# Kernel optimization log

Hardware: AMD Instinct MI355X
Metric: run time of the kernel (lower is better)

The kernel has to match this reference:

```python
import jax, jax.numpy as jnp
import numpy as np

V, T, NS, NH, E, H = 4, 4, 100000, 12288, 100000, 64
NEG_SLOPE = 0.01  # nn.LeakyReLU default


def setup_inputs() -> dict:
    key = jax.random.key(0)
    k1, k2, k3, k4, k5 = jax.random.split(key, 5)
    x = jax.random.normal(k1, (V, T, NS), dtype=jnp.float32)          # per-var, per-t scalar node features
    src_idx = jax.random.randint(k2, (V, T, E), 0, NS, dtype=jnp.int32)
    dst_idx = jax.random.randint(k3, (V, T, E), 0, NH, dtype=jnp.int32)
    W = jax.random.normal(k4, (V, T, H), dtype=jnp.float32)            # GraphConv weight, in_feats=1 -> [1,H] per etype
    b = jax.random.normal(k5, (V, T, H), dtype=jnp.float32) * 0.02     # GraphConv bias per etype
    return {"x": x, "W": W, "b": b, "src_idx": src_idx, "dst_idx": dst_idx, "n_healpix": NH}


def reference(x, W, b, src_idx, dst_idx, n_healpix):
    # x: [V,T,NS]; W,b: [V,T,H]; src_idx,dst_idx: [V,T,E]
    x = jnp.nan_to_num(x, nan=0.0)

    def conv_scalar(x_v, src, dst):
        # x_v: [T,NS] (all timestep features for this var), src/dst: [E] for ONE edge type
        ones = jnp.ones(src.shape, x_v.dtype)
        deg_out = jax.ops.segment_sum(ones, src, num_segments=NS)       # out-degree of src nodes
        deg_in = jax.ops.segment_sum(ones, dst, num_segments=n_healpix)  # in-degree of dst nodes
        norm_src = jax.lax.rsqrt(jnp.maximum(deg_out, 1.0))
        norm_dst = jax.lax.rsqrt(jnp.maximum(deg_in, 1.0))
        msg = x_v[:, src] * norm_src[src]                                # [T,E] gather
        agg = jax.vmap(lambda m: jax.ops.segment_sum(m, dst, num_segments=n_healpix))(msg)  # [T,NH]
        return agg * norm_dst                                            # norm='both'

    # HeteroGraphConv bug-faithful: for each var, EVERY per-t' conv is applied to each x[:,t]
    # s[v, t', t, n] = normalized scatter of x[v,t] through edges of etype t'
    s = jax.vmap(lambda xv, sv, dv: jax.vmap(lambda se, de: conv_scalar(xv, se, de))(sv, dv))(
        x, src_idx, dst_idx)                                             # [V,T',T,NH]

    # in_feats=1: linear is outer product with W row; bias + LeakyReLU inside each conv, sum over etypes t'
    h = jax.nn.leaky_relu(s[..., None] * W[:, :, None, None, :] + b[:, :, None, None, :],
                          negative_slope=NEG_SLOPE)                      # [V,T',T,NH,H]
    out = h.sum(axis=1)                                                  # aggregate='sum' over edge types -> [V,T,NH,H]
    # final stacking: stack over t (dim=1) then over vars (dim=1) -> [NH, V, T, H]
    return jnp.transpose(out, (2, 0, 1, 3))
```

## Files before the change

### kernel.cpp

```cpp
#include <hip/hip_runtime.h>
#include <math.h>

#define V    4
#define T    4
#define NSRC 100000
#define NHX  12288
#define E    100000
#define H    64
#define VT   16

#define SL    16
#define SLE   (E/SL)
#define HF    8
#define HE    (E/HF)
#define CW    (NSRC/8)
#define LDSW  12500
#define NCH   12
#define NPB   8

#define S1_TRANS  391
#define S1_CNT    (HF*VT)
#define S1_DHIST  (SL*VT)
#define S2_SCAN   (NCH*VT)
#define S2_NSFIN  ((VT*CW + 1023)/1024)

typedef float vf4 __attribute__((ext_vector_type(4)));

__global__ void __launch_bounds__(1024)
s1_kernel(const float* __restrict__ x, const int* __restrict__ src,
          const int* __restrict__ dst, float4* __restrict__ x4,
          unsigned int* __restrict__ cnt_part, unsigned char* __restrict__ ph8,
          unsigned int* __restrict__ cs) {
    __shared__ unsigned int lds[LDSW];
    const int b = blockIdx.x, tid = threadIdx.x;

    if (b < S1_TRANS) {
        const int g = b * 1024 + tid;
        if (g < V * NSRC) {
            const int v = g / NSRC, s = g - v * NSRC;
            const float* xr = x + (size_t)v * T * NSRC + s;
            float a0 = xr[0], a1 = xr[NSRC], a2 = xr[2 * NSRC], a3 = xr[3 * NSRC];
            float4 r;
            r.x = (a0 == a0) ? a0 : 0.0f;
            r.y = (a1 == a1) ? a1 : 0.0f;
            r.z = (a2 == a2) ? a2 : 0.0f;
            r.w = (a3 == a3) ? a3 : 0.0f;
            x4[g] = r;
        }
        return;
    }
    if (b < S1_TRANS + S1_CNT) {
        const int idx = b - S1_TRANS;
        const int hf = idx & 7;
        const int vt = idx >> 3;
        for (int i = tid; i < CW; i += 1024) lds[i] = 0u;
        __syncthreads();
        const int* s_row = src + vt * E + hf * HE;
        for (int e = tid; e < HE; e += 1024) {
            const unsigned r = (unsigned)s_row[e];
            atomicAdd(&lds[r >> 3], 1u << ((r & 7) * 4));
        }
        __syncthreads();
        unsigned int* outp = cnt_part + ((size_t)hf * VT + vt) * CW;
        for (int i = tid; i < CW; i += 1024) outp[i] = lds[i];
        return;
    }
    {
        const int idx = b - (S1_TRANS + S1_CNT);
        const int sl = idx & 15, vt = idx >> 4;
        for (int i = tid; i < NHX; i += 1024) lds[i] = 0u;
        __syncthreads();
        const int* d_row = dst + vt * E + sl * SLE;
        for (int e = tid; e < SLE; e += 1024)
            atomicAdd(&lds[d_row[e]], 1u);
        __syncthreads();
        unsigned char* outp = ph8 + ((size_t)vt * SL + sl) * NHX;
        for (int i = tid; i < NHX; i += 1024)
            outp[i] = (unsigned char)lds[i];
        const int lane = tid & 63, wv = tid >> 6;
        if (wv < NCH) {
            unsigned int s = 0;
#pragma unroll
            for (int i = 0; i < 16; ++i) s += lds[wv * 1024 + i * 64 + lane];
#pragma unroll
            for (int off = 32; off > 0; off >>= 1)
                s += (unsigned int)__shfl_down((int)s, off, 64);
            if (lane == 0) cs[((size_t)vt * SL + sl) * NCH + wv] = s;
        }
    }
}

__global__ void __launch_bounds__(1024)
s2_kernel(const unsigned int* __restrict__ cnt_part,
          const unsigned char* __restrict__ ph8,
          const unsigned int* __restrict__ cs,
          float4* __restrict__ ns4,
          unsigned char* __restrict__ pre8,
          unsigned int* __restrict__ colstart) {
    const int b = blockIdx.x, tid = threadIdx.x;

    if (b < S2_SCAN) {
        const int vt = b & 15, ch = b >> 4;
        const int lane = tid & 63, wv = tid >> 6;
        const int d = ch * 1024 + tid;
        __shared__ unsigned int wsum[16];
        __shared__ unsigned int sbase;
        if (wv == 0) {
            unsigned int p = 0;
            if (lane < SL)
                for (int c = 0; c < ch; ++c)
                    p += cs[((size_t)vt * SL + lane) * NCH + c];
#pragma unroll
            for (int off = 8; off > 0; off >>= 1)
                p += (unsigned int)__shfl_down((int)p, off, 64);
            if (lane == 0) sbase = p;
        }
        unsigned int h[SL];
        unsigned int tot = 0;
#pragma unroll
        for (int s = 0; s < SL; ++s) {
            h[s] = (unsigned int)ph8[((size_t)vt * SL + s) * NHX + d];
            tot += h[s];
        }
        unsigned int incl = tot;
#pragma unroll
        for (int off = 1; off < 64; off <<= 1) {
            const unsigned int vup = (unsigned int)__shfl_up((int)incl, off, 64);
            if (lane >= off) incl += vup;
        }
        if (lane == 63) wsum[wv] = incl;
        __syncthreads();
        if (tid == 0) {
            unsigned int run = sbase;
#pragma unroll
            for (int w = 0; w < 16; ++w) { const unsigned int t2 = wsum[w]; wsum[w] = run; run += t2; }
        }
        __syncthreads();
        const unsigned int excl = wsum[wv] + (incl - tot);
        const size_t vd = (size_t)vt * NHX + d;
        colstart[vd] = excl | (tot << 20);
        unsigned int acc = 0;
#pragma unroll
        for (int s = 0; s < SL; ++s) {
            pre8[((size_t)vt * SL + s) * NHX + d] = (unsigned char)acc;
            acc += h[s];
        }
        return;
    }
    {
        const int g = (b - S2_SCAN) * 1024 + tid;
        if (g >= VT * CW) return;
        unsigned slo = 0, shi = 0;
#pragma unroll
        for (int hf = 0; hf < HF; ++hf) {
            const unsigned w = cnt_part[(size_t)hf * (VT * CW) + g];
            slo += w & 0x0F0F0F0Fu;
            shi += (w >> 4) & 0x0F0F0F0Fu;
        }
        float4 r0, r1;
        r0.x = rsqrtf(fmaxf((float)(slo & 0xFFu), 1.0f));
        r0.y = rsqrtf(fmaxf((float)(shi & 0xFFu), 1.0f));
        r0.z = rsqrtf(fmaxf((float)((slo >> 8) & 0xFFu), 1.0f));
        r0.w = rsqrtf(fmaxf((float)((shi >> 8) & 0xFFu), 1.0f));
        r1.x = rsqrtf(fmaxf((float)((slo >> 16) & 0xFFu), 1.0f));
        r1.y = rsqrtf(fmaxf((float)((shi >> 16) & 0xFFu), 1.0f));
        r1.z = rsqrtf(fmaxf((float)(slo >> 24), 1.0f));
        r1.w = rsqrtf(fmaxf((float)(shi >> 24), 1.0f));
        ns4[2 * (size_t)g]     = r0;
        ns4[2 * (size_t)g + 1] = r1;
    }
}

__global__ void __launch_bounds__(1024)
s3_reorder(const int* __restrict__ src, const int* __restrict__ dst,
           const unsigned int* __restrict__ colstart,
           const unsigned char* __restrict__ pre8,
           int* __restrict__ sorted) {
    const int b = blockIdx.x;
    const int k = b & 7, j = b >> 3;
    const int vt = 2 * k + (j & 1);
    const int sl = j >> 1;
    __shared__ unsigned int pos[NHX];
    const unsigned int*  cst = colstart + (size_t)vt * NHX;
    const unsigned char* pr  = pre8 + ((size_t)vt * SL + sl) * NHX;
    for (int i = threadIdx.x; i < NHX; i += 1024)
        pos[i] = (cst[i] & 0xFFFFFu) + (unsigned int)pr[i];
    __syncthreads();
    const int* s_row = src + vt * E + sl * SLE;
    const int* d_row = dst + vt * E + sl * SLE;
    int* outp = sorted + (size_t)vt * E;
    for (int e = threadIdx.x; e < SLE; e += 1024) {
        const int d = d_row[e];
        const int s = s_row[e];
        const unsigned int p = atomicAdd(&pos[d], 1u);
        outp[p] = s;
    }
}

__global__ void __launch_bounds__(256)
s4_accum(const float4* __restrict__ x4, const int* __restrict__ sorted,
         const float* __restrict__ ns,
         const unsigned int* __restrict__ colstart,
         float4* __restrict__ sval) {
    const int b = blockIdx.x;
    const int k = b & 7, j = b >> 3;
    const int vt = 2 * k + (j & 1);
    const int chunk = j >> 1;
    const int d = chunk * 64 + (threadIdx.x >> 2);
    const int q = threadIdx.x & 3;
    const int v = vt >> 2;
    const size_t vd = (size_t)vt * NHX + d;
    const unsigned int pk   = colstart[vd];
    const unsigned int base = pk & 0xFFFFFu;
    const unsigned int deg  = pk >> 20;
    const int*    srt    = sorted + (size_t)vt * E;
    const float*  ns_row = ns + (size_t)vt * NSRC;
    const float4* x_row  = x4 + (size_t)v * NSRC;
    float4 acc = make_float4(0.f, 0.f, 0.f, 0.f);
    for (unsigned int i = q; i < deg; i += 4) {
        const int s = srt[base + i];
        const float4 xa = x_row[s];
        const float  na = ns_row[s];
        acc.x += xa.x * na; acc.y += xa.y * na;
        acc.z += xa.z * na; acc.w += xa.w * na;
    }
    acc.x += __shfl_xor(acc.x, 1, 64);
    acc.y += __shfl_xor(acc.y, 1, 64);
    acc.z += __shfl_xor(acc.z, 1, 64);
    acc.w += __shfl_xor(acc.w, 1, 64);
    acc.x += __shfl_xor(acc.x, 2, 64);
    acc.y += __shfl_xor(acc.y, 2, 64);
    acc.z += __shfl_xor(acc.z, 2, 64);
    acc.w += __shfl_xor(acc.w, 2, 64);
    if (q == 0) {
        const float nd = rsqrtf(fmaxf((float)deg, 1.0f));
        acc.x *= nd; acc.y *= nd; acc.z *= nd; acc.w *= nd;
        sval[vd] = acc;
    }
}

__global__ void __launch_bounds__(256)
s5_epilogue(const float4* __restrict__ sval, const float* __restrict__ Wm,
            const float* __restrict__ bm, float* __restrict__ out) {
    const int n0  = blockIdx.x * NPB;
    const int tid = threadIdx.x;
    __shared__ float sW[VT * H];
    __shared__ float sb[VT * H];
    __shared__ float sv[VT][T][NPB];

    for (int i = tid; i < VT * H; i += 256) { sW[i] = Wm[i]; sb[i] = bm[i]; }
    if (tid < VT * NPB) {
        const int vt = tid >> 3, n = tid & 7;
        const float4 r = sval[(size_t)vt * NHX + n0 + n];
        sv[vt][0][n] = r.x; sv[vt][1][n] = r.y;
        sv[vt][2][n] = r.z; sv[vt][3][n] = r.w;
    }
    __syncthreads();

    const int v  = tid >> 6;
    const int t  = (tid >> 4) & 3;
    const int hb = (tid & 15) * 4;
    float4 Wr[4], Br[4];
#pragma unroll
    for (int tp = 0; tp < 4; ++tp) {
        const int wi = (v * 4 + tp) * H + hb;
        Wr[tp] = *(const float4*)&sW[wi];
        Br[tp] = *(const float4*)&sb[wi];
    }
#pragma unroll
    for (int n = 0; n < NPB; ++n) {
        float4 o = make_float4(0.f, 0.f, 0.f, 0.f);
#pragma unroll
        for (int tp = 0; tp < 4; ++tp) {
            const float s = sv[v * 4 + tp][t][n];
            float a;
            a = fmaf(s, Wr[tp].x, Br[tp].x); o.x += (a > 0.f) ? a : 0.01f * a;
            a = fmaf(s, Wr[tp].y, Br[tp].y); o.y += (a > 0.f) ? a : 0.01f * a;
            a = fmaf(s, Wr[tp].z, Br[tp].z); o.z += (a > 0.f) ? a : 0.01f * a;
            a = fmaf(s, Wr[tp].w, Br[tp].w); o.w += (a > 0.f) ? a : 0.01f * a;
        }
        vf4* dstp = (vf4*)(out + (size_t)(n0 + n) * (V * T * H)) + tid;
        __builtin_nontemporal_store(*(vf4*)&o, dstp);
    }
}

extern "C" void kernel_launch(void* const* d_in, const int* in_sizes, int n_in,
                              void* d_out, int out_size, void* d_ws, size_t ws_size,
                              hipStream_t stream) {
    const float* x   = (const float*)d_in[0];
    const float* Wm  = (const float*)d_in[1];
    const float* bm  = (const float*)d_in[2];
    const int*   src = (const int*)d_in[3];
    const int*   dst = (const int*)d_in[4];
    float* out = (float*)d_out;

    char* ws = (char*)d_ws;
    size_t off = 0;
    float4* x4 = (float4*)(ws + off);                   off += (size_t)V * NSRC * 16;
    float4* sval = (float4*)(ws + off);                 off += (size_t)VT * NHX * 16;
    float4* ns4 = (float4*)(ws + off);                  off += (size_t)VT * NSRC * 4;
    unsigned char* ph8 = (unsigned char*)(ws + off);    off += (size_t)VT * SL * NHX;
    unsigned char* pre8 = (unsigned char*)(ws + off);   off += (size_t)VT * SL * NHX;
    unsigned int* colstart = (unsigned int*)(ws + off); off += (size_t)VT * NHX * 4;
    unsigned int* cs = (unsigned int*)(ws + off);       off += (size_t)VT * SL * NCH * 4;
    unsigned int* cnt_part = (unsigned int*)(ws + off); off += (size_t)HF * VT * CW * 4;
    int* sorted = (int*)(ws + off);                     off += (size_t)VT * E * 4;
    float* ns = (float*)ns4;

    s1_kernel<<<S1_TRANS + S1_CNT + S1_DHIST, 1024, 0, stream>>>(
        x, src, dst, x4, cnt_part, ph8, cs);
    s2_kernel<<<S2_SCAN + S2_NSFIN, 1024, 0, stream>>>(
        cnt_part, ph8, cs, ns4, pre8, colstart);
    s3_reorder<<<SL * VT, 1024, 0, stream>>>(src, dst, colstart, pre8, sorted);
    s4_accum<<<3072, 256, 0, stream>>>(x4, sorted, ns, colstart, sval);
    s5_epilogue<<<NHX / NPB, 256, 0, stream>>>(sval, Wm, bm, out);
}
```

Measured before the change: 139.9 us.

## Fuse gather-accumulate into epilogue kernel and halve out-degree histogram split

```diff
diff --git a/kernel.cpp b/kernel.cpp
--- a/kernel.cpp
+++ b/kernel.cpp
@@ -11,7 +11,7 @@
 
 #define SL    16
 #define SLE   (E/SL)
-#define HF    8
+#define HF    4
 #define HE    (E/HF)
 #define CW    (NSRC/8)
 #define LDSW  12500
@@ -51,8 +51,8 @@
     }
     if (b < S1_TRANS + S1_CNT) {
         const int idx = b - S1_TRANS;
-        const int hf = idx & 7;
-        const int vt = idx >> 3;
+        const int hf = idx & 3;
+        const int vt = idx >> 2;
         for (int i = tid; i < CW; i += 1024) lds[i] = 0u;
         __syncthreads();
         const int* s_row = src + vt * E + hf * HE;
@@ -197,69 +197,62 @@
     }
 }
 
-__global__ void __launch_bounds__(256)
-s4_accum(const float4* __restrict__ x4, const int* __restrict__ sorted,
-         const float* __restrict__ ns,
-         const unsigned int* __restrict__ colstart,
-         float4* __restrict__ sval) {
-    const int b = blockIdx.x;
-    const int k = b & 7, j = b >> 3;
-    const int vt = 2 * k + (j & 1);
-    const int chunk = j >> 1;
-    const int d = chunk * 64 + (threadIdx.x >> 2);
-    const int q = threadIdx.x & 3;
-    const int v = vt >> 2;
-    const size_t vd = (size_t)vt * NHX + d;
-    const unsigned int pk   = colstart[vd];
-    const unsigned int base = pk & 0xFFFFFu;
-    const unsigned int deg  = pk >> 20;
-    const int*    srt    = sorted + (size_t)vt * E;
-    const float*  ns_row = ns + (size_t)vt * NSRC;
-    const float4* x_row  = x4 + (size_t)v * NSRC;
-    float4 acc = make_float4(0.f, 0.f, 0.f, 0.f);
-    for (unsigned int i = q; i < deg; i += 4) {
-        const int s = srt[base + i];
-        const float4 xa = x_row[s];
-        const float  na = ns_row[s];
-        acc.x += xa.x * na; acc.y += xa.y * na;
-        acc.z += xa.z * na; acc.w += xa.w * na;
-    }
-    acc.x += __shfl_xor(acc.x, 1, 64);
-    acc.y += __shfl_xor(acc.y, 1, 64);
-    acc.z += __shfl_xor(acc.z, 1, 64);
-    acc.w += __shfl_xor(acc.w, 1, 64);
-    acc.x += __shfl_xor(acc.x, 2, 64);
-    acc.y += __shfl_xor(acc.y, 2, 64);
-    acc.z += __shfl_xor(acc.z, 2, 64);
-    acc.w += __shfl_xor(acc.w, 2, 64);
-    if (q == 0) {
-        const float nd = rsqrtf(fmaxf((float)deg, 1.0f));
-        acc.x *= nd; acc.y *= nd; acc.z *= nd; acc.w *= nd;
-        sval[vd] = acc;
-    }
-}
-
-__global__ void __launch_bounds__(256)
-s5_epilogue(const float4* __restrict__ sval, const float* __restrict__ Wm,
-            const float* __restrict__ bm, float* __restrict__ out) {
+__global__ void __launch_bounds__(512)
+s45_kernel(const float4* __restrict__ x4, const int* __restrict__ sorted,
+           const float* __restrict__ ns,
+           const unsigned int* __restrict__ colstart,
+           const float* __restrict__ Wm, const float* __restrict__ bm,
+           float* __restrict__ out) {
     const int n0  = blockIdx.x * NPB;
     const int tid = threadIdx.x;
     __shared__ float sW[VT * H];
     __shared__ float sb[VT * H];
     __shared__ float sv[VT][T][NPB];
 
-    for (int i = tid; i < VT * H; i += 256) { sW[i] = Wm[i]; sb[i] = bm[i]; }
-    if (tid < VT * NPB) {
-        const int vt = tid >> 3, n = tid & 7;
-        const float4 r = sval[(size_t)vt * NHX + n0 + n];
-        sv[vt][0][n] = r.x; sv[vt][1][n] = r.y;
-        sv[vt][2][n] = r.z; sv[vt][3][n] = r.w;
+    for (int i = tid; i < VT * H; i += 512) { sW[i] = Wm[i]; sb[i] = bm[i]; }
+
+    {
+        const int seg = tid >> 2;
+        const int q   = tid & 3;
+        const int vt  = seg >> 3;
+        const int n   = seg & 7;
+        const int v   = vt >> 2;
+        const size_t vd = (size_t)vt * NHX + (n0 + n);
+        const unsigned int pk   = colstart[vd];
+        const unsigned int base = pk & 0xFFFFFu;
+        const unsigned int deg  = pk >> 20;
+        const int*    srt    = sorted + (size_t)vt * E;
+        const float*  ns_row = ns + (size_t)vt * NSRC;
+        const float4* x_row  = x4 + (size_t)v * NSRC;
+        float4 acc = make_float4(0.f, 0.f, 0.f, 0.f);
+        for (unsigned int i = q; i < deg; i += 4) {
+            const int s = srt[base + i];
+            const float4 xa = x_row[s];
+            const float  na = ns_row[s];
+            acc.x += xa.x * na; acc.y += xa.y * na;
+            acc.z += xa.z * na; acc.w += xa.w * na;
+        }
+        acc.x += __shfl_xor(acc.x, 1, 64);
+        acc.y += __shfl_xor(acc.y, 1, 64);
+        acc.z += __shfl_xor(acc.z, 1, 64);
+        acc.w += __shfl_xor(acc.w, 1, 64);
+        acc.x += __shfl_xor(acc.x, 2, 64);
+        acc.y += __shfl_xor(acc.y, 2, 64);
+        acc.z += __shfl_xor(acc.z, 2, 64);
+        acc.w += __shfl_xor(acc.w, 2, 64);
+        if (q == 0) {
+            const float nd = rsqrtf(fmaxf((float)deg, 1.0f));
+            sv[vt][0][n] = acc.x * nd; sv[vt][1][n] = acc.y * nd;
+            sv[vt][2][n] = acc.z * nd; sv[vt][3][n] = acc.w * nd;
+        }
     }
     __syncthreads();
 
-    const int v  = tid >> 6;
-    const int t  = (tid >> 4) & 3;
-    const int hb = (tid & 15) * 4;
+    const int lt = tid & 255;
+    const int nh = tid >> 8;
+    const int v  = lt >> 6;
+    const int t  = (lt >> 4) & 3;
+    const int hb = (lt & 15) * 4;
     float4 Wr[4], Br[4];
 #pragma unroll
     for (int tp = 0; tp < 4; ++tp) {
@@ -268,7 +261,8 @@
         Br[tp] = *(const float4*)&sb[wi];
     }
 #pragma unroll
-    for (int n = 0; n < NPB; ++n) {
+    for (int np = 0; np < NPB; np += 2) {
+        const int n = np + nh;
         float4 o = make_float4(0.f, 0.f, 0.f, 0.f);
 #pragma unroll
         for (int tp = 0; tp < 4; ++tp) {
@@ -279,7 +273,7 @@
             a = fmaf(s, Wr[tp].z, Br[tp].z); o.z += (a > 0.f) ? a : 0.01f * a;
             a = fmaf(s, Wr[tp].w, Br[tp].w); o.w += (a > 0.f) ? a : 0.01f * a;
         }
-        vf4* dstp = (vf4*)(out + (size_t)(n0 + n) * (V * T * H)) + tid;
+        vf4* dstp = (vf4*)(out + (size_t)(n0 + n) * (V * T * H)) + lt;
         __builtin_nontemporal_store(*(vf4*)&o, dstp);
     }
 }
@@ -297,7 +291,6 @@
     char* ws = (char*)d_ws;
     size_t off = 0;
     float4* x4 = (float4*)(ws + off);                   off += (size_t)V * NSRC * 16;
-    float4* sval = (float4*)(ws + off);                 off += (size_t)VT * NHX * 16;
     float4* ns4 = (float4*)(ws + off);                  off += (size_t)VT * NSRC * 4;
     unsigned char* ph8 = (unsigned char*)(ws + off);    off += (size_t)VT * SL * NHX;
     unsigned char* pre8 = (unsigned char*)(ws + off);   off += (size_t)VT * SL * NHX;
@@ -312,6 +305,5 @@
     s2_kernel<<<S2_SCAN + S2_NSFIN, 1024, 0, stream>>>(
         cnt_part, ph8, cs, ns4, pre8, colstart);
     s3_reorder<<<SL * VT, 1024, 0, stream>>>(src, dst, colstart, pre8, sorted);
-    s4_accum<<<3072, 256, 0, stream>>>(x4, sorted, ns, colstart, sval);
-    s5_epilogue<<<NHX / NPB, 256, 0, stream>>>(sval, Wm, bm, out);
-}
+    s45_kernel<<<NHX / NPB, 512, 0, stream>>>(x4, sorted, ns, colstart, Wm, bm, out);
+}
```

Result: slower. 165.4 us (+18.2%).
